# Performance work log

Hardware: AMD Instinct MI355X
Metric: run time of the kernel (lower is better)

Reference implementation:

```python
import jax, jax.numpy as jnp
import numpy as np

QMAX = 127.0  # 2**(bits-1) - 1 for bits=8, signed symmetric


def _quantize_signed_symmetric(t):
    # per-tensor symmetric: scale = max|t| / qmax, q = clamp(round(t/scale))
    scale = jnp.max(jnp.abs(t)) / QMAX
    q = jnp.clip(jnp.round(t / scale), -QMAX, QMAX)
    return q, scale


def setup_inputs() -> dict:
    key = jax.random.key(0)
    k1, k2, k3 = jax.random.split(key, 3)
    N, D_IN, D_OUT = 16384, 1024, 1024
    x = jax.random.normal(k1, (N, D_IN), dtype=jnp.float32)
    weight = jax.random.normal(k2, (D_OUT, D_IN), dtype=jnp.float32) * 0.02
    bias = jax.random.normal(k3, (D_OUT,), dtype=jnp.float32) * 0.01
    return {"x": x, "weight": weight, "bias": bias}


def reference(x, weight, bias):
    # weight quantization (cached in torch; recomputed here, same math)
    qw, w_scale = _quantize_signed_symmetric(weight)
    qw_t = qw.astype(jnp.int32).T            # [D_IN, D_OUT]
    # activation quantization
    qx, x_scale = _quantize_signed_symmetric(x)
    qx = qx.astype(jnp.int32)                # [N, D_IN]
    # int32 matmul, then per-tensor dequant + bias
    acc = qx @ qw_t                          # int32 [N, D_OUT]
    y = acc.astype(jnp.float32) * (x_scale * w_scale)
    return y + bias
```

## Files before the change

kernel.cpp:

```cpp
#include <hip/hip_runtime.h>

#define QMAX 127.0f
#define BM 128
#define BN 128
#define BK 64

typedef int int4v __attribute__((ext_vector_type(4)));

__global__ void absmax2_kernel(const float4* __restrict__ px, int n4x,
                               const float4* __restrict__ pw, int n4w,
                               int gx, int* __restrict__ amax) {
    const float4* p; int n4; int* out; int nb, bid;
    if ((int)blockIdx.x < gx) { p = px; n4 = n4x; out = amax + 0; nb = gx; bid = blockIdx.x; }
    else { p = pw; n4 = n4w; out = amax + 1; nb = gridDim.x - gx; bid = blockIdx.x - gx; }
    float m = 0.f;
    int stride = nb * blockDim.x;
    for (int i = bid * blockDim.x + threadIdx.x; i < n4; i += stride) {
        float4 v = p[i];
        m = fmaxf(m, fmaxf(fmaxf(fabsf(v.x), fabsf(v.y)),
                           fmaxf(fabsf(v.z), fabsf(v.w))));
    }
    for (int off = 32; off; off >>= 1) m = fmaxf(m, __shfl_down(m, off, 64));
    __shared__ float sm[4];
    if ((threadIdx.x & 63) == 0) sm[threadIdx.x >> 6] = m;
    __syncthreads();
    if (threadIdx.x == 0) {
        float b = fmaxf(fmaxf(sm[0], sm[1]), fmaxf(sm[2], sm[3]));
        atomicMax(out, (int)__float_as_uint(b));
    }
}

__device__ __forceinline__ int qone(float v, float s) {
    float q = fminf(fmaxf(rintf(v / s), -QMAX), QMAX);
    return (int)q;
}
__device__ __forceinline__ int qpack4(float4 v, float s) {
    return (qone(v.x, s) & 255) | ((qone(v.y, s) & 255) << 8) |
           ((qone(v.z, s) & 255) << 16) | ((qone(v.w, s) & 255) << 24);
}

__global__ void quant2_kernel(const float4* __restrict__ sx, int4v* __restrict__ dx, int n16x,
                              const float4* __restrict__ sw, int4v* __restrict__ dw, int n16w,
                              int gx, const int* __restrict__ amax) {
    const float4* src; int4v* dst; int n16, nb, bid; float scale;
    if ((int)blockIdx.x < gx) {
        src = sx; dst = dx; n16 = n16x; nb = gx; bid = blockIdx.x;
        scale = __uint_as_float((unsigned)amax[0]) / QMAX;
    } else {
        src = sw; dst = dw; n16 = n16w; nb = gridDim.x - gx; bid = blockIdx.x - gx;
        scale = __uint_as_float((unsigned)amax[1]) / QMAX;
    }
    int stride = nb * blockDim.x;
    for (int i = bid * blockDim.x + threadIdx.x; i < n16; i += stride) {
        float4 v0 = src[4 * i + 0];
        float4 v1 = src[4 * i + 1];
        float4 v2 = src[4 * i + 2];
        float4 v3 = src[4 * i + 3];
        int4v o = { qpack4(v0, scale), qpack4(v1, scale),
                    qpack4(v2, scale), qpack4(v3, scale) };
        dst[i] = o;
    }
}

typedef const __attribute__((address_space(1))) char glob_char;
typedef __attribute__((address_space(3))) char lds_char;

__device__ __forceinline__ void gload16(const char* g, char* l) {
    __builtin_amdgcn_global_load_lds((glob_char*)g, (lds_char*)l, 16, 0, 0);
}

__global__ __launch_bounds__(256, 4) void gemm_i8_kernel(
        const char* __restrict__ qa, const char* __restrict__ qb,
        const float* __restrict__ bias, const int* __restrict__ amax,
        float* __restrict__ out, int M, int N, int K, int nbx) {
    __shared__ char sA[BM * BK];
    __shared__ char sB[BN * BK];

    const int b = blockIdx.x;
    const int chunk = gridDim.x >> 3;
    const int s = (b & 7) * chunk + (b >> 3);
    const int mt = s / nbx, nt = s % nbx;

    const int tid = threadIdx.x;
    const int lane = tid & 63;
    const int wid = tid >> 6;
    const int wm = wid >> 1, wn = wid & 1;
    const int m0 = mt * BM, n0 = nt * BN;

    const int L0 = tid, L1 = 256 + tid;
    const int row0 = ((L0 >> 6) << 4) + (L0 & 15);
    const int col0 = ((L0 >> 4) & 3) << 4;
    const int row1 = ((L1 >> 6) << 4) + (L1 & 15);
    const int col1 = ((L1 >> 4) & 3) << 4;

    const char* gA0 = qa + (size_t)(m0 + row0) * K + col0;
    const char* gA1 = qa + (size_t)(m0 + row1) * K + col1;
    const char* gB0 = qb + (size_t)(n0 + row0) * K + col0;
    const char* gB1 = qb + (size_t)(n0 + row1) * K + col1;
    char* lA0 = sA + L0 * 16;
    char* lA1 = sA + L1 * 16;
    char* lB0 = sB + L0 * 16;
    char* lB1 = sB + L1 * 16;

    int4v acc[4][4];
    const int4v zero = {0, 0, 0, 0};
#pragma unroll
    for (int i = 0; i < 4; ++i)
#pragma unroll
        for (int j = 0; j < 4; ++j) acc[i][j] = zero;

    const int4v* sAv = (const int4v*)sA;
    const int4v* sBv = (const int4v*)sB;
    const int aoff = wm * 4 * 64 + lane;
    const int boff = wn * 4 * 64 + lane;

    for (int k0 = 0; k0 < K; k0 += BK) {
        gload16(gA0, lA0);
        gload16(gA1, lA1);
        gload16(gB0, lB0);
        gload16(gB1, lB1);
        gA0 += BK; gA1 += BK; gB0 += BK; gB1 += BK;
        __syncthreads();

        int4v a[4], bfr[4];
#pragma unroll
        for (int t = 0; t < 4; ++t) {
            a[t] = sAv[aoff + t * 64];
            bfr[t] = sBv[boff + t * 64];
        }
#pragma unroll
        for (int i = 0; i < 4; ++i)
#pragma unroll
            for (int j = 0; j < 4; ++j)
                acc[i][j] = __builtin_amdgcn_mfma_i32_16x16x64_i8(a[i], bfr[j], acc[i][j], 0, 0, 0);
        __syncthreads();
    }

    const float sc = (__uint_as_float((unsigned)amax[0]) / QMAX) *
                     (__uint_as_float((unsigned)amax[1]) / QMAX);
    const int cbase = n0 + wn * 64 + (lane & 15);
    const int rbase = m0 + wm * 64 + ((lane >> 4) << 2);
#pragma unroll
    for (int j = 0; j < 4; ++j) {
        const int col = cbase + j * 16;
        const float bv = bias[col];
#pragma unroll
        for (int i = 0; i < 4; ++i) {
            const int row = rbase + i * 16;
#pragma unroll
            for (int r = 0; r < 4; ++r) {
                out[(size_t)(row + r) * N + col] = (float)acc[i][j][r] * sc + bv;
            }
        }
    }
}

extern "C" void kernel_launch(void* const* d_in, const int* in_sizes, int n_in,
                              void* d_out, int out_size, void* d_ws, size_t ws_size,
                              hipStream_t stream) {
    const float* x = (const float*)d_in[0];
    const float* w = (const float*)d_in[1];
    const float* bias = (const float*)d_in[2];
    float* out = (float*)d_out;

    const int xn = in_sizes[0];
    const int wn = in_sizes[1];
    const int N = in_sizes[2];
    const int K = wn / N;
    const int M = xn / K;

    int* amax = (int*)d_ws;
    char* qx = (char*)d_ws + 1024;
    char* qw = qx + (size_t)M * K;

    const int GAX = 2048, GAW = 256;
    absmax2_kernel<<<GAX + GAW, 256, 0, stream>>>(
        (const float4*)x, xn / 4, (const float4*)w, wn / 4, GAX, amax);

    const int GQX = 4096, GQW = 256;
    quant2_kernel<<<GQX + GQW, 256, 0, stream>>>(
        (const float4*)x, (int4v*)qx, xn / 16,
        (const float4*)w, (int4v*)qw, wn / 16, GQX, amax);

    const int nbx = N / BN;
    gemm_i8_kernel<<<nbx * (M / BM), 256, 0, stream>>>(qx, qw, bias, amax, out, M, N, K, nbx);
}
```

Baseline: 181.5 us.

## Double-buffer LDS tiles in int8 GEMM to overlap global loads with MFMA

Splits the A and B shared-memory tiles into two buffers. The next K-slice is prefetched with global_load_lds into the alternate buffer while MFMAs run on the current one, which also drops the trailing barrier so each iteration has a single __syncthreads. This is meant to hide global-load latency in the GEMM main loop. In exchange, LDS use per block doubles, which can limit how many blocks fit on a CU, and correctness relies on the barrier waiting for the outstanding LDS-direct loads.

```diff
diff --git a/kernel.cpp b/kernel.cpp
--- a/kernel.cpp
+++ b/kernel.cpp
@@ -73,8 +73,8 @@
         const char* __restrict__ qa, const char* __restrict__ qb,
         const float* __restrict__ bias, const int* __restrict__ amax,
         float* __restrict__ out, int M, int N, int K, int nbx) {
-    __shared__ char sA[BM * BK];
-    __shared__ char sB[BN * BK];
+    __shared__ char sA[2][BM * BK];
+    __shared__ char sB[2][BN * BK];
 
     const int b = blockIdx.x;
     const int chunk = gridDim.x >> 3;
@@ -97,10 +97,6 @@
     const char* gA1 = qa + (size_t)(m0 + row1) * K + col1;
     const char* gB0 = qb + (size_t)(n0 + row0) * K + col0;
     const char* gB1 = qb + (size_t)(n0 + row1) * K + col1;
-    char* lA0 = sA + L0 * 16;
-    char* lA1 = sA + L1 * 16;
-    char* lB0 = sB + L0 * 16;
-    char* lB1 = sB + L1 * 16;
 
     int4v acc[4][4];
     const int4v zero = {0, 0, 0, 0};
@@ -109,19 +105,31 @@
 #pragma unroll
         for (int j = 0; j < 4; ++j) acc[i][j] = zero;
 
-    const int4v* sAv = (const int4v*)sA;
-    const int4v* sBv = (const int4v*)sB;
     const int aoff = wm * 4 * 64 + lane;
     const int boff = wn * 4 * 64 + lane;
+    const int NI = K / BK;
 
-    for (int k0 = 0; k0 < K; k0 += BK) {
-        gload16(gA0, lA0);
-        gload16(gA1, lA1);
-        gload16(gB0, lB0);
-        gload16(gB1, lB1);
-        gA0 += BK; gA1 += BK; gB0 += BK; gB1 += BK;
+    gload16(gA0, sA[0] + L0 * 16);
+    gload16(gA1, sA[0] + L1 * 16);
+    gload16(gB0, sB[0] + L0 * 16);
+    gload16(gB1, sB[0] + L1 * 16);
+    gA0 += BK; gA1 += BK; gB0 += BK; gB1 += BK;
+
+    for (int k0 = 0; k0 < NI; ++k0) {
+        const int cur = k0 & 1;
         __syncthreads();
 
+        if (k0 + 1 < NI) {
+            const int nxt = cur ^ 1;
+            gload16(gA0, sA[nxt] + L0 * 16);
+            gload16(gA1, sA[nxt] + L1 * 16);
+            gload16(gB0, sB[nxt] + L0 * 16);
+            gload16(gB1, sB[nxt] + L1 * 16);
+            gA0 += BK; gA1 += BK; gB0 += BK; gB1 += BK;
+        }
+
+        const int4v* sAv = (const int4v*)sA[cur];
+        const int4v* sBv = (const int4v*)sB[cur];
         int4v a[4], bfr[4];
 #pragma unroll
         for (int t = 0; t < 4; ++t) {
@@ -133,7 +141,6 @@
 #pragma unroll
             for (int j = 0; j < 4; ++j)
                 acc[i][j] = __builtin_amdgcn_mfma_i32_16x16x64_i8(a[i], bfr[j], acc[i][j], 0, 0, 0);
-        __syncthreads();
     }
 
     const float sc = (__uint_as_float((unsigned)amax[0]) / QMAX) *
```

After: 181.2 us. No clear change (-0.1%).

## Load MFMA fragments directly from global memory with register double-buffering

Applied to the files above, without the earlier changes.

Removes the LDS staging and both block barriers from the int8 GEMM main loop. Each lane now loads its MFMA fragments straight from global memory. Two sets of fragment registers are alternated so the next k-slice loads while the current one runs on MFMA. This gives up LDS data sharing between waves, since each wave reloads its own A/B rows and L2/global traffic goes up, and register pressure rises, so launch bounds drop to 3 blocks per CU. The loop assumes K/64 is even and at least 2.

```diff
diff --git a/kernel.cpp b/kernel.cpp
--- a/kernel.cpp
+++ b/kernel.cpp
@@ -3,7 +3,6 @@
 #define QMAX 127.0f
 #define BM 128
 #define BN 128
-#define BK 64
 
 typedef int int4v __attribute__((ext_vector_type(4)));
 
@@ -62,45 +61,30 @@
     }
 }
 
-typedef const __attribute__((address_space(1))) char glob_char;
-typedef __attribute__((address_space(3))) char lds_char;
-
-__device__ __forceinline__ void gload16(const char* g, char* l) {
-    __builtin_amdgcn_global_load_lds((glob_char*)g, (lds_char*)l, 16, 0, 0);
-}
-
-__global__ __launch_bounds__(256, 4) void gemm_i8_kernel(
+__global__ __launch_bounds__(256, 3) void gemm_i8_kernel(
         const char* __restrict__ qa, const char* __restrict__ qb,
         const float* __restrict__ bias, const int* __restrict__ amax,
         float* __restrict__ out, int M, int N, int K, int nbx) {
-    __shared__ char sA[BM * BK];
-    __shared__ char sB[BN * BK];
-
     const int b = blockIdx.x;
     const int chunk = gridDim.x >> 3;
     const int s = (b & 7) * chunk + (b >> 3);
     const int mt = s / nbx, nt = s % nbx;
 
-    const int tid = threadIdx.x;
-    const int lane = tid & 63;
-    const int wid = tid >> 6;
+    const int lane = threadIdx.x & 63;
+    const int wid = threadIdx.x >> 6;
     const int wm = wid >> 1, wn = wid & 1;
     const int m0 = mt * BM, n0 = nt * BN;
 
-    const int L0 = tid, L1 = 256 + tid;
-    const int row0 = ((L0 >> 6) << 4) + (L0 & 15);
-    const int col0 = ((L0 >> 4) & 3) << 4;
-    const int row1 = ((L1 >> 6) << 4) + (L1 & 15);
-    const int col1 = ((L1 >> 4) & 3) << 4;
+    const int rlane = lane & 15;
+    const int koff = (lane >> 4) << 4;
 
-    const char* gA0 = qa + (size_t)(m0 + row0) * K + col0;
-    const char* gA1 = qa + (size_t)(m0 + row1) * K + col1;
-    const char* gB0 = qb + (size_t)(n0 + row0) * K + col0;
-    const char* gB1 = qb + (size_t)(n0 + row1) * K + col1;
-    char* lA0 = sA + L0 * 16;
-    char* lA1 = sA + L1 * 16;
-    char* lB0 = sB + L0 * 16;
-    char* lB1 = sB + L1 * 16;
+    const char* pa[4];
+    const char* pb[4];
+#pragma unroll
+    for (int t = 0; t < 4; ++t) {
+        pa[t] = qa + (size_t)(m0 + wm * 64 + t * 16 + rlane) * K + koff;
+        pb[t] = qb + (size_t)(n0 + wn * 64 + t * 16 + rlane) * K + koff;
+    }
 
     int4v acc[4][4];
     const int4v zero = {0, 0, 0, 0};
@@ -109,32 +93,36 @@
 #pragma unroll
         for (int j = 0; j < 4; ++j) acc[i][j] = zero;
 
-    const int4v* sAv = (const int4v*)sA;
-    const int4v* sBv = (const int4v*)sB;
-    const int aoff = wm * 4 * 64 + lane;
-    const int boff = wn * 4 * 64 + lane;
+#define LOADF(Ab, Bb)                                   \
+    do {                                                \
+        _Pragma("unroll") for (int t = 0; t < 4; ++t) { \
+            Ab[t] = *(const int4v*)pa[t];               \
+            Bb[t] = *(const int4v*)pb[t];               \
+            pa[t] += 64; pb[t] += 64;                   \
+        }                                               \
+    } while (0)
+#define MFMAF(Ab, Bb)                                                       \
+    do {                                                                    \
+        _Pragma("unroll") for (int i = 0; i < 4; ++i)                       \
+            _Pragma("unroll") for (int j = 0; j < 4; ++j)                   \
+                acc[i][j] = __builtin_amdgcn_mfma_i32_16x16x64_i8(          \
+                    Ab[i], Bb[j], acc[i][j], 0, 0, 0);                      \
+    } while (0)
 
-    for (int k0 = 0; k0 < K; k0 += BK) {
-        gload16(gA0, lA0);
-        gload16(gA1, lA1);
-        gload16(gB0, lB0);
-        gload16(gB1, lB1);
-        gA0 += BK; gA1 += BK; gB0 += BK; gB1 += BK;
-        __syncthreads();
+    int4v A0[4], B0[4], A1[4], B1[4];
+    const int NI = K >> 6;
 
-        int4v a[4], bfr[4];
-#pragma unroll
-        for (int t = 0; t < 4; ++t) {
-            a[t] = sAv[aoff + t * 64];
-            bfr[t] = sBv[boff + t * 64];
-        }
-#pragma unroll
-        for (int i = 0; i < 4; ++i)
-#pragma unroll
-            for (int j = 0; j < 4; ++j)
-                acc[i][j] = __builtin_amdgcn_mfma_i32_16x16x64_i8(a[i], bfr[j], acc[i][j], 0, 0, 0);
-        __syncthreads();
+    LOADF(A0, B0);
+#pragma unroll 1
+    for (int k = 0; k < NI - 2; k += 2) {
+        LOADF(A1, B1);
+        MFMAF(A0, B0);
+        LOADF(A0, B0);
+        MFMAF(A1, B1);
     }
+    LOADF(A1, B1);
+    MFMAF(A0, B0);
+    MFMAF(A1, B1);
 
     const float sc = (__uint_as_float((unsigned)amax[0]) / QMAX) *
                      (__uint_as_float((unsigned)amax[1]) / QMAX);
```

Result: slower. 204.3 us (+12.6%).
